# Kernel tuning notes

Measured on AMD Instinct MI355X. Metric: run time of the kernel, lower is better.

## Reference

```python
import jax, jax.numpy as jnp
import numpy as np

NUM_HEADS = 16
BLOCK_SIZE = 64


def setup_inputs() -> dict:
    key = jax.random.key(0)
    ks = jax.random.split(key, 5)
    B, S, C = 2, 2047, 1024
    return {
        "x": jax.random.normal(ks[0], (B, S, C), dtype=jnp.float32),
        "global_token": jax.random.normal(ks[1], (1, 1, C), dtype=jnp.float32),
        "qkv_w": jax.random.normal(ks[2], (3 * C, C), dtype=jnp.float32) * 0.02,
        "proj_w": jax.random.normal(ks[3], (C, C), dtype=jnp.float32) * 0.02,
        "proj_b": jax.random.normal(ks[4], (C,), dtype=jnp.float32) * 0.02,
    }


def reference(x, global_token, qkv_w, proj_w, proj_b):
    B, S, C = x.shape
    H = NUM_HEADS
    D = C // H
    scale = D ** -0.5
    # prepend global token -> N = S + 1
    g = jnp.broadcast_to(global_token, (B, 1, C))
    xg = jnp.concatenate([g, x], axis=1)
    N = S + 1
    # fused qkv projection (torch Linear: x @ W^T)
    qkv = (xg @ qkv_w.T).reshape(B, N, 3, H, D)
    qkv = jnp.transpose(qkv, (2, 0, 3, 1, 4))  # [3, B, H, N, D]
    q, k, v = qkv[0], qkv[1], qkv[2]
    # block-causal mask: query t sees key j iff block(j) <= block(t)
    blk = jnp.arange(N) // BLOCK_SIZE
    mask = blk[:, None] >= blk[None, :]  # [N, N]
    attn = jnp.einsum("bhqd,bhkd->bhqk", q, k) * scale
    attn = jnp.where(mask[None, None], attn, -jnp.inf)
    attn = jax.nn.softmax(attn, axis=-1)
    out = jnp.einsum("bhqk,bhkd->bhqd", attn, v)
    out = jnp.transpose(out, (0, 2, 1, 3)).reshape(B, N, C)
    out = out[:, 1:, :]  # drop global token
    return out @ proj_w.T + proj_b
```

## Files before the change

kernel.cpp:

```cpp
#include <hip/hip_runtime.h>
#include <math.h>

typedef _Float16 h16;
typedef _Float16 half8 __attribute__((ext_vector_type(8)));
typedef _Float16 half4 __attribute__((ext_vector_type(4)));
typedef float f32x4 __attribute__((ext_vector_type(4)));

#define NB 2
#define NS 2047
#define NC 1024
#define NN 2048
#define NH 16
#define ND 64

__device__ __forceinline__ void gl_lds16(const h16* g, h16* l) {
  __builtin_amdgcn_global_load_lds((const __attribute__((address_space(1))) void*)g,
                                   (__attribute__((address_space(3))) void*)l, 16, 0, 0);
}
__device__ __forceinline__ f32x4 mfma32(half8 a, half8 b, f32x4 c) {
  return __builtin_amdgcn_mfma_f32_16x16x32_f16(a, b, c, 0, 0, 0);
}
__device__ __forceinline__ f32x4 mfma16x(half4 a, half4 b, f32x4 c) {
  return __builtin_amdgcn_mfma_f32_16x16x16f16(a, b, c, 0, 0, 0);
}

__global__ __launch_bounds__(256) void cast_all_k(
    const float* __restrict__ x, const float* __restrict__ g,
    const float* __restrict__ qw, const float* __restrict__ pw, h16* __restrict__ out) {
  const size_t i = ((size_t)blockIdx.x * 256 + threadIdx.x) * 8;
  const float* src;
  if (i < (size_t)NB * NN * NC) {
    const int c = (int)(i & (NC - 1));
    const int n = (int)((i >> 10) & (NN - 1));
    const int b = (int)(i >> 21);
    src = (n == 0) ? (g + c) : (x + ((size_t)b * NS + (n - 1)) * NC + c);
  } else {
    const size_t j = i - (size_t)NB * NN * NC;
    src = (j < (size_t)3 * NC * NC) ? (qw + j) : (pw + (j - (size_t)3 * NC * NC));
  }
  float4 f0 = ((const float4*)src)[0];
  float4 f1 = ((const float4*)src)[1];
  h16 tmp[8];
  tmp[0] = (h16)f0.x; tmp[1] = (h16)f0.y; tmp[2] = (h16)f0.z; tmp[3] = (h16)f0.w;
  tmp[4] = (h16)f1.x; tmp[5] = (h16)f1.y; tmp[6] = (h16)f1.z; tmp[7] = (h16)f1.w;
  *(half8*)(out + i) = *(half8*)&tmp[0];
}

__global__ __launch_bounds__(256, 6) void gemm_qkv_h(
    const h16* __restrict__ A, const h16* __restrict__ W,
    h16* __restrict__ qP, h16* __restrict__ kP, h16* __restrict__ vP) {
  __shared__ h16 SM[64 * 64 + 128 * 64];
  h16* As = SM;
  h16* Bs = SM + 64 * 64;
  const int tid = threadIdx.x;
  const int flat = blockIdx.y * 24 + blockIdx.x;
  const int swz = (flat & 7) * 192 + (flat >> 3);
  const int m0 = (swz / 24) * 64, j0 = (swz % 24) * 128;
  const int wid = tid >> 6, lane = tid & 63, l15 = lane & 15, quad = lane >> 4;
  const int wr = wid >> 1, wc = wid & 1;
  const int rl = lane >> 3, csw = (lane & 7) ^ rl;
  const h16* ag0 = A + (size_t)(m0 + wid * 16 + rl) * NC + csw * 8;
  const h16* ag1 = A + (size_t)(m0 + wid * 16 + 8 + rl) * NC + csw * 8;
  const h16* bg = W + (size_t)(j0 + wid * 32 + rl) * NC + csw * 8;
  f32x4 acc[2][4];
#pragma unroll
  for (int rt = 0; rt < 2; ++rt)
#pragma unroll
    for (int ct = 0; ct < 4; ++ct) acc[rt][ct] = (f32x4){0.f, 0.f, 0.f, 0.f};

  for (int k0 = 0; k0 < NC; k0 += 64) {
    __syncthreads();
    gl_lds16(ag0 + k0, &As[(wid * 16) * 64]);
    gl_lds16(ag1 + k0, &As[(wid * 16 + 8) * 64]);
#pragma unroll
    for (int i = 0; i < 4; ++i)
      gl_lds16(bg + (size_t)i * 8 * NC + k0, &Bs[(wid * 32 + i * 8) * 64]);
    __syncthreads();
#pragma unroll
    for (int ks = 0; ks < 2; ++ks) {
      const int p0 = ((ks * 4 + quad) ^ (l15 & 7)) * 8;
      half8 af[2], bf[4];
#pragma unroll
      for (int rt = 0; rt < 2; ++rt)
        af[rt] = *(const half8*)&As[(wr * 32 + rt * 16 + l15) * 64 + p0];
#pragma unroll
      for (int ct = 0; ct < 4; ++ct)
        bf[ct] = *(const half8*)&Bs[(wc * 64 + ct * 16 + l15) * 64 + p0];
#pragma unroll
      for (int rt = 0; rt < 2; ++rt)
#pragma unroll
        for (int ct = 0; ct < 4; ++ct)
          acc[rt][ct] = mfma32(af[rt], bf[ct], acc[rt][ct]);
    }
  }

  const int b = m0 >> 11, n0 = m0 & (NN - 1);
  if (j0 < 2 * NC) {
    h16* base = (j0 < NC) ? qP : kP;
    const int coff = (j0 < NC) ? 0 : NC;
    const int h = (j0 - coff + wc * 64) >> 6;
    h16* dst = base + ((size_t)(b * NH + h) * NN + n0) * ND;
#pragma unroll
    for (int rt = 0; rt < 2; ++rt)
#pragma unroll
      for (int ct = 0; ct < 4; ++ct)
#pragma unroll
        for (int r = 0; r < 4; ++r) {
          const int mloc = wr * 32 + rt * 16 + quad * 4 + r;
          dst[(size_t)mloc * ND + ct * 16 + l15] = (h16)acc[rt][ct][r];
        }
  } else {
    __syncthreads();
#pragma unroll
    for (int rt = 0; rt < 2; ++rt)
#pragma unroll
      for (int ct = 0; ct < 4; ++ct)
#pragma unroll
        for (int r = 0; r < 4; ++r) {
          const int mloc = wr * 32 + rt * 16 + quad * 4 + r;
          const int jloc = wc * 64 + ct * 16 + l15;
          SM[mloc * 128 + (jloc ^ (((mloc >> 2) & 3) << 3))] = (h16)acc[rt][ct][r];
        }
    __syncthreads();
    const int kb0 = n0 >> 6;
    const int h0 = (j0 - 2 * NC) >> 6;
    const int w = tid >> 6, d = tid & 63;
#pragma unroll
    for (int u = 0; u < 2; ++u) {
      const int bh = b * NH + h0 + u;
      h16 buf[16];
#pragma unroll
      for (int kk = 0; kk < 16; ++kk) {
        const int row = w * 16 + kk;
        buf[kk] = SM[row * 128 + ((u * 64 + d) ^ (((row >> 2) & 3) << 3))];
      }
      h16* dstv = vP + ((size_t)((bh * 32 + kb0) * 4 + w)) * 1024 + d * 16;
      *(half8*)dstv = *(half8*)&buf[0];
      *(half8*)(dstv + 8) = *(half8*)&buf[8];
    }
  }
}

__global__ __launch_bounds__(256, 3) void attn_h(
    const h16* __restrict__ qP, const h16* __restrict__ kP,
    const h16* __restrict__ vP, h16* __restrict__ outp) {
  __shared__ float RED[2 * 64 * 36];
  __shared__ float DEN[4 * 64];
  const int bx = blockIdx.x;
  const int qb = 31 - (bx >> 5);
  const int bh = bx & 31;
  const int b = bh >> 4, h = bh & 15;
  const int tid = threadIdx.x, w = tid >> 6, lane = tid & 63;
  const int l15 = lane & 15, quad = lane >> 4;

  half8 bq[4][2];
#pragma unroll
  for (int nt = 0; nt < 4; ++nt) {
    const h16* qp = qP + ((size_t)bh * NN + qb * 64 + nt * 16 + l15) * ND + quad * 8;
    bq[nt][0] = (*(const half8*)qp) * (h16)0.125f;
    bq[nt][1] = (*(const half8*)(qp + 32)) * (h16)0.125f;
  }
  const h16* kbase = kP + ((size_t)bh * NN + w * 16 + l15) * ND + quad * 8;
  const h16* vbase = vP + ((size_t)bh * 32 * 4 + w) * 1024 + l15 * 16 + quad * 4;

  f32x4 o[4][4];
  float den[4] = {0.f, 0.f, 0.f, 0.f};
#pragma unroll
  for (int mt = 0; mt < 4; ++mt)
#pragma unroll
    for (int nt = 0; nt < 4; ++nt) o[mt][nt] = (f32x4){0.f, 0.f, 0.f, 0.f};

  half8 kf0 = *(const half8*)kbase;
  half8 kf1 = *(const half8*)(kbase + 32);
  half4 vf0 = *(const half4*)(vbase);
  half4 vf1 = *(const half4*)(vbase + 256);
  half4 vf2 = *(const half4*)(vbase + 512);
  half4 vf3 = *(const half4*)(vbase + 768);

  for (int kb = 0; kb <= qb; ++kb) {
    const int nkb = (kb < qb) ? kb + 1 : kb;
    const h16* kn = kbase + (size_t)nkb * 64 * ND;
    const h16* vn = vbase + (size_t)nkb * 4096;
    half8 nk0 = *(const half8*)kn;
    half8 nk1 = *(const half8*)(kn + 32);
    half4 nv0 = *(const half4*)(vn);
    half4 nv1 = *(const half4*)(vn + 256);
    half4 nv2 = *(const half4*)(vn + 512);
    half4 nv3 = *(const half4*)(vn + 768);
    __builtin_amdgcn_s_setprio(1);
#pragma unroll
    for (int nt = 0; nt < 4; ++nt) {
      f32x4 s = (f32x4){0.f, 0.f, 0.f, 0.f};
      s = mfma32(kf0, bq[nt][0], s);
      s = mfma32(kf1, bq[nt][1], s);
      float e0 = __expf(s[0]), e1 = __expf(s[1]);
      float e2 = __expf(s[2]), e3 = __expf(s[3]);
      den[nt] += (e0 + e1) + (e2 + e3);
      int2 pi;
      pi.x = __builtin_bit_cast(int, __builtin_amdgcn_cvt_pkrtz(e0, e1));
      pi.y = __builtin_bit_cast(int, __builtin_amdgcn_cvt_pkrtz(e2, e3));
      half4 p = __builtin_bit_cast(half4, pi);
      o[0][nt] = mfma16x(vf0, p, o[0][nt]);
      o[1][nt] = mfma16x(vf1, p, o[1][nt]);
      o[2][nt] = mfma16x(vf2, p, o[2][nt]);
      o[3][nt] = mfma16x(vf3, p, o[3][nt]);
    }
    __builtin_amdgcn_s_setprio(0);
    kf0 = nk0; kf1 = nk1;
    vf0 = nv0; vf1 = nv1; vf2 = nv2; vf3 = nv3;
  }

#pragma unroll
  for (int nt = 0; nt < 4; ++nt) {
    den[nt] += __shfl_xor(den[nt], 16);
    den[nt] += __shfl_xor(den[nt], 32);
  }
  __syncthreads();
  if (quad == 0) {
#pragma unroll
    for (int nt = 0; nt < 4; ++nt) DEN[w * 64 + nt * 16 + l15] = den[nt];
  }
#pragma unroll
  for (int r = 0; r < 2; ++r) {
    if (r) __syncthreads();
    if (w < 2) {
#pragma unroll
      for (int mt2 = 0; mt2 < 2; ++mt2)
#pragma unroll
        for (int nt = 0; nt < 4; ++nt)
          *(f32x4*)&RED[(w * 64 + nt * 16 + l15) * 36 + mt2 * 16 + quad * 4] =
              o[r * 2 + mt2][nt];
    }
    __syncthreads();
    if (w >= 2) {
#pragma unroll
      for (int mt2 = 0; mt2 < 2; ++mt2)
#pragma unroll
        for (int nt = 0; nt < 4; ++nt) {
          float* p = &RED[((w - 2) * 64 + nt * 16 + l15) * 36 + mt2 * 16 + quad * 4];
          f32x4 t = *(f32x4*)p;
          *(f32x4*)p = t + o[r * 2 + mt2][nt];
        }
    }
    __syncthreads();
    {
      const int q = w * 16 + l15;
      const float dt = DEN[q] + DEN[64 + q] + DEN[128 + q] + DEN[192 + q];
      const float inv = 1.f / dt;
      f32x4 x0 = *(const f32x4*)&RED[(0 * 64 + q) * 36 + quad * 8];
      f32x4 x1 = *(const f32x4*)&RED[(0 * 64 + q) * 36 + quad * 8 + 4];
      f32x4 y0 = *(const f32x4*)&RED[(1 * 64 + q) * 36 + quad * 8];
      f32x4 y1 = *(const f32x4*)&RED[(1 * 64 + q) * 36 + quad * 8 + 4];
      x0 += y0;
      x1 += y1;
      int4 pk;
      pk.x = __builtin_bit_cast(int, __builtin_amdgcn_cvt_pkrtz(x0[0] * inv, x0[1] * inv));
      pk.y = __builtin_bit_cast(int, __builtin_amdgcn_cvt_pkrtz(x0[2] * inv, x0[3] * inv));
      pk.z = __builtin_bit_cast(int, __builtin_amdgcn_cvt_pkrtz(x1[0] * inv, x1[1] * inv));
      pk.w = __builtin_bit_cast(int, __builtin_amdgcn_cvt_pkrtz(x1[2] * inv, x1[3] * inv));
      h16* op = outp + (size_t)(b * NN + qb * 64 + q) * NC + h * ND + r * 32 + quad * 8;
      *(half8*)op = __builtin_bit_cast(half8, pk);
    }
  }
}

__global__ __launch_bounds__(256) void gemm_proj_h(
    const h16* __restrict__ Ah, const h16* __restrict__ W,
    const float* __restrict__ bias, float* __restrict__ out) {
  __shared__ h16 As[64 * 64];
  __shared__ h16 Bs[128 * 64];
  const int tid = threadIdx.x;
  const int flat = blockIdx.y * 8 + blockIdx.x;
  const int swz = (flat & 7) * 64 + (flat >> 3);
  const int m0 = (swz >> 3) * 64, j0 = (swz & 7) * 128;
  const int wid = tid >> 6, lane = tid & 63, l15 = lane & 15, quad = lane >> 4;
  const int wr = wid >> 1, wc = wid & 1;
  const int rl = lane >> 3, csw = (lane & 7) ^ rl;
  const h16* ag[2];
#pragma unroll
  for (int i = 0; i < 2; ++i) {
    int m = m0 + wid * 16 + i * 8 + rl;
    if (m > NB * NS - 1) m = NB * NS - 1;
    const int bb = (m >= NS) ? 1 : 0;
    ag[i] = Ah + (size_t)(bb * NN + m - bb * NS + 1) * NC + csw * 8;
  }
  const h16* bg = W + (size_t)(j0 + wid * 32 + rl) * NC + csw * 8;
  f32x4 acc[2][4];
#pragma unroll
  for (int rt = 0; rt < 2; ++rt)
#pragma unroll
    for (int ct = 0; ct < 4; ++ct) acc[rt][ct] = (f32x4){0.f, 0.f, 0.f, 0.f};

  for (int k0 = 0; k0 < NC; k0 += 64) {
    __syncthreads();
    gl_lds16(ag[0] + k0, &As[(wid * 16) * 64]);
    gl_lds16(ag[1] + k0, &As[(wid * 16 + 8) * 64]);
#pragma unroll
    for (int i = 0; i < 4; ++i)
      gl_lds16(bg + (size_t)i * 8 * NC + k0, &Bs[(wid * 32 + i * 8) * 64]);
    __syncthreads();
#pragma unroll
    for (int ks = 0; ks < 2; ++ks) {
      const int p0 = ((ks * 4 + quad) ^ (l15 & 7)) * 8;
      half8 af[2], bf[4];
#pragma unroll
      for (int rt = 0; rt < 2; ++rt)
        af[rt] = *(const half8*)&As[(wr * 32 + rt * 16 + l15) * 64 + p0];
#pragma unroll
      for (int ct = 0; ct < 4; ++ct)
        bf[ct] = *(const half8*)&Bs[(wc * 64 + ct * 16 + l15) * 64 + p0];
#pragma unroll
      for (int rt = 0; rt < 2; ++rt)
#pragma unroll
        for (int ct = 0; ct < 4; ++ct)
          acc[rt][ct] = mfma32(af[rt], bf[ct], acc[rt][ct]);
    }
  }
#pragma unroll
  for (int ct = 0; ct < 4; ++ct) {
    const float bv = bias[j0 + wc * 64 + ct * 16 + l15];
#pragma unroll
    for (int rt = 0; rt < 2; ++rt)
#pragma unroll
      for (int r = 0; r < 4; ++r) {
        const int mm = m0 + wr * 32 + rt * 16 + quad * 4 + r;
        if (mm < NB * NS)
          out[(size_t)mm * NC + j0 + wc * 64 + ct * 16 + l15] = acc[rt][ct][r] + bv;
      }
  }
}

extern "C" void kernel_launch(void* const* d_in, const int* in_sizes, int n_in,
                              void* d_out, int out_size, void* d_ws, size_t ws_size,
                              hipStream_t stream) {
  const float* x = (const float*)d_in[0];
  const float* g = (const float*)d_in[1];
  const float* qkv_w = (const float*)d_in[2];
  const float* proj_w = (const float*)d_in[3];
  const float* proj_b = (const float*)d_in[4];
  float* out = (float*)d_out;

  h16* xgh  = (h16*)d_ws;
  h16* w3h  = xgh + (size_t)NB * NN * NC;
  h16* wph  = w3h + (size_t)3 * NC * NC;
  h16* qP   = wph + (size_t)NC * NC;
  h16* kP   = qP + (size_t)NB * NH * NN * ND;
  h16* vP   = kP + (size_t)NB * NH * NN * ND;
  h16* attnh = vP + (size_t)NB * NH * NN * ND;

  cast_all_k<<<dim3(4096), 256, 0, stream>>>(x, g, qkv_w, proj_w, xgh);
  gemm_qkv_h<<<dim3(24, 64), 256, 0, stream>>>(xgh, w3h, qP, kP, vP);
  attn_h<<<dim3(1024), 256, 0, stream>>>(qP, kP, vP, attnh);
  gemm_proj_h<<<dim3(8, 64), 256, 0, stream>>>(attnh, wph, proj_b, out);
}
```

Measured before the change: 173.6 us.

## Restructure QKV GEMM into 256x256 tiles with double-buffered LDS pipeline

Rewrites the QKV projection GEMM from 64x128 tiles on 256 threads to 256x256 tiles on 512 threads, with each wave computing a 128x64 sub-tile. K-slices of 32 are double-buffered in LDS, and the next slice is prefetched with global_load_lds interleaved between MFMA groups, using manual vmcnt waits, raw barriers and setprio. The goal is higher arithmetic intensity and overlap of loads with compute. In exchange the grid shrinks to 192 blocks, which may underfill the 256 CUs, and register pressure from 128 accumulator floats per thread rises. The V transpose epilogue is reworked in two passes through LDS.

```diff
diff --git a/kernel.cpp b/kernel.cpp
--- a/kernel.cpp
+++ b/kernel.cpp
@@ -46,97 +46,129 @@
   *(half8*)(out + i) = *(half8*)&tmp[0];
 }
 
-__global__ __launch_bounds__(256, 6) void gemm_qkv_h(
+__global__ __launch_bounds__(512, 2) void gemm_qkv_h(
     const h16* __restrict__ A, const h16* __restrict__ W,
     h16* __restrict__ qP, h16* __restrict__ kP, h16* __restrict__ vP) {
-  __shared__ h16 SM[64 * 64 + 128 * 64];
-  h16* As = SM;
-  h16* Bs = SM + 64 * 64;
+  __shared__ h16 SM[32768];
   const int tid = threadIdx.x;
-  const int flat = blockIdx.y * 24 + blockIdx.x;
-  const int swz = (flat & 7) * 192 + (flat >> 3);
-  const int m0 = (swz / 24) * 64, j0 = (swz % 24) * 128;
+  const int flat = blockIdx.y * 12 + blockIdx.x;
+  const int swz = (flat & 7) * 24 + (flat >> 3);
+  const int m0 = (swz / 12) * 256, j0 = (swz % 12) * 256;
   const int wid = tid >> 6, lane = tid & 63, l15 = lane & 15, quad = lane >> 4;
-  const int wr = wid >> 1, wc = wid & 1;
-  const int rl = lane >> 3, csw = (lane & 7) ^ rl;
-  const h16* ag0 = A + (size_t)(m0 + wid * 16 + rl) * NC + csw * 8;
-  const h16* ag1 = A + (size_t)(m0 + wid * 16 + 8 + rl) * NC + csw * 8;
-  const h16* bg = W + (size_t)(j0 + wid * 32 + rl) * NC + csw * 8;
-  f32x4 acc[2][4];
-#pragma unroll
-  for (int rt = 0; rt < 2; ++rt)
-#pragma unroll
-    for (int ct = 0; ct < 4; ++ct) acc[rt][ct] = (f32x4){0.f, 0.f, 0.f, 0.f};
-
-  for (int k0 = 0; k0 < NC; k0 += 64) {
-    __syncthreads();
-    gl_lds16(ag0 + k0, &As[(wid * 16) * 64]);
-    gl_lds16(ag1 + k0, &As[(wid * 16 + 8) * 64]);
-#pragma unroll
-    for (int i = 0; i < 4; ++i)
-      gl_lds16(bg + (size_t)i * 8 * NC + k0, &Bs[(wid * 32 + i * 8) * 64]);
-    __syncthreads();
-#pragma unroll
-    for (int ks = 0; ks < 2; ++ks) {
-      const int p0 = ((ks * 4 + quad) ^ (l15 & 7)) * 8;
-      half8 af[2], bf[4];
-#pragma unroll
-      for (int rt = 0; rt < 2; ++rt)
-        af[rt] = *(const half8*)&As[(wr * 32 + rt * 16 + l15) * 64 + p0];
-#pragma unroll
-      for (int ct = 0; ct < 4; ++ct)
-        bf[ct] = *(const half8*)&Bs[(wc * 64 + ct * 16 + l15) * 64 + p0];
-#pragma unroll
-      for (int rt = 0; rt < 2; ++rt)
-#pragma unroll
-        for (int ct = 0; ct < 4; ++ct)
-          acc[rt][ct] = mfma32(af[rt], bf[ct], acc[rt][ct]);
-    }
+  const int wm = wid >> 2, wn = wid & 3;
+
+  const int glin = (lane & 7) ^ (lane >> 3);
+  const int rowoff = glin >> 2, kg = glin & 3;
+  const int srow = (wid * 8 + (lane >> 3)) * 2 + rowoff;
+  const h16* ag = A + (size_t)(m0 + srow) * NC + kg * 8;
+  const h16* bg = W + (size_t)(j0 + srow) * NC + kg * 8;
+
+  const int rsw = l15 >> 1;
+  const int gs = (((l15 & 1) << 2) | quad) ^ rsw;
+  const int aoff = wm * 4096 + rsw * 64 + gs * 8;
+  const int boff = wn * 2048 + rsw * 64 + gs * 8;
+
+  f32x4 acc[8][4];
+#pragma unroll
+  for (int fm = 0; fm < 8; ++fm)
+#pragma unroll
+    for (int fn = 0; fn < 4; ++fn) acc[fm][fn] = (f32x4){0.f, 0.f, 0.f, 0.f};
+
+  gl_lds16(ag, &SM[(wid * 8) * 64]);
+  gl_lds16(ag + (size_t)128 * NC, &SM[(64 + wid * 8) * 64]);
+  gl_lds16(bg, &SM[16384 + (wid * 8) * 64]);
+  gl_lds16(bg + (size_t)128 * NC, &SM[16384 + (64 + wid * 8) * 64]);
+
+  for (int kt = 0; kt < 32; ++kt) {
+    const int cur = kt & 1, nxt = cur ^ 1;
+    const int k1 = (kt + 1) * 32;
+    const bool pre = (kt < 31);
+    const h16* Ab = SM + cur * 8192;
+    const h16* Bb = SM + 16384 + cur * 8192;
+
+    if (pre) {
+      gl_lds16(ag + k1, &SM[nxt * 8192 + (wid * 8) * 64]);
+      gl_lds16(ag + (size_t)128 * NC + k1, &SM[nxt * 8192 + (64 + wid * 8) * 64]);
+      asm volatile("s_waitcnt vmcnt(2)" ::: "memory");
+    } else {
+      asm volatile("s_waitcnt vmcnt(0)" ::: "memory");
+    }
+    asm volatile("s_barrier" ::: "memory");
+
+    half8 bf[4];
+#pragma unroll
+    for (int fn = 0; fn < 4; ++fn) bf[fn] = *(const half8*)&Bb[boff + fn * 512];
+
+#pragma unroll
+    for (int q = 0; q < 4; ++q) {
+      if (q == 1 && pre)
+        gl_lds16(bg + k1, &SM[16384 + nxt * 8192 + (wid * 8) * 64]);
+      if (q == 2 && pre)
+        gl_lds16(bg + (size_t)128 * NC + k1, &SM[16384 + nxt * 8192 + (64 + wid * 8) * 64]);
+      half8 af0 = *(const half8*)&Ab[aoff + (q * 2 + 0) * 512];
+      half8 af1 = *(const half8*)&Ab[aoff + (q * 2 + 1) * 512];
+      __builtin_amdgcn_s_setprio(1);
+#pragma unroll
+      for (int fn = 0; fn < 4; ++fn) {
+        acc[q * 2 + 0][fn] = mfma32(af0, bf[fn], acc[q * 2 + 0][fn]);
+        acc[q * 2 + 1][fn] = mfma32(af1, bf[fn], acc[q * 2 + 1][fn]);
+      }
+      __builtin_amdgcn_s_setprio(0);
+    }
+    asm volatile("s_barrier" ::: "memory");
   }
 
   const int b = m0 >> 11, n0 = m0 & (NN - 1);
   if (j0 < 2 * NC) {
     h16* base = (j0 < NC) ? qP : kP;
     const int coff = (j0 < NC) ? 0 : NC;
-    const int h = (j0 - coff + wc * 64) >> 6;
+    const int h = (j0 - coff + wn * 64) >> 6;
     h16* dst = base + ((size_t)(b * NH + h) * NN + n0) * ND;
 #pragma unroll
-    for (int rt = 0; rt < 2; ++rt)
-#pragma unroll
-      for (int ct = 0; ct < 4; ++ct)
+    for (int fm = 0; fm < 8; ++fm)
+#pragma unroll
+      for (int fn = 0; fn < 4; ++fn)
 #pragma unroll
         for (int r = 0; r < 4; ++r) {
-          const int mloc = wr * 32 + rt * 16 + quad * 4 + r;
-          dst[(size_t)mloc * ND + ct * 16 + l15] = (h16)acc[rt][ct][r];
+          const int mloc = wm * 128 + fm * 16 + quad * 4 + r;
+          dst[(size_t)mloc * ND + fn * 16 + l15] = (h16)acc[fm][fn][r];
         }
   } else {
-    __syncthreads();
-#pragma unroll
-    for (int rt = 0; rt < 2; ++rt)
-#pragma unroll
-      for (int ct = 0; ct < 4; ++ct)
-#pragma unroll
-        for (int r = 0; r < 4; ++r) {
-          const int mloc = wr * 32 + rt * 16 + quad * 4 + r;
-          const int jloc = wc * 64 + ct * 16 + l15;
-          SM[mloc * 128 + (jloc ^ (((mloc >> 2) & 3) << 3))] = (h16)acc[rt][ct][r];
-        }
-    __syncthreads();
     const int kb0 = n0 >> 6;
     const int h0 = (j0 - 2 * NC) >> 6;
-    const int w = tid >> 6, d = tid & 63;
-#pragma unroll
-    for (int u = 0; u < 2; ++u) {
-      const int bh = b * NH + h0 + u;
-      h16 buf[16];
-#pragma unroll
-      for (int kk = 0; kk < 16; ++kk) {
-        const int row = w * 16 + kk;
-        buf[kk] = SM[row * 128 + ((u * 64 + d) ^ (((row >> 2) & 3) << 3))];
+    const int g = tid >> 6, d = tid & 63;
+    __syncthreads();
+#pragma unroll
+    for (int p = 0; p < 2; ++p) {
+      if (p) __syncthreads();
+      if (wm == p) {
+#pragma unroll
+        for (int fm = 0; fm < 8; ++fm)
+#pragma unroll
+          for (int fn = 0; fn < 4; ++fn)
+#pragma unroll
+            for (int r = 0; r < 4; ++r) {
+              const int lrow = fm * 16 + quad * 4 + r;
+              const int col = wn * 64 + fn * 16 + l15;
+              SM[lrow * 256 + (col ^ ((lrow & 7) << 3))] = (h16)acc[fm][fn][r];
+            }
       }
-      h16* dstv = vP + ((size_t)((bh * 32 + kb0) * 4 + w)) * 1024 + d * 16;
-      *(half8*)dstv = *(half8*)&buf[0];
-      *(half8*)(dstv + 8) = *(half8*)&buf[8];
+      __syncthreads();
+#pragma unroll
+      for (int u = 0; u < 4; ++u) {
+        const int idx = g * 4 + u;
+        const int kbl2 = idx >> 4, hl = (idx >> 2) & 3, w4 = idx & 3;
+        const int bh = b * NH + h0 + hl;
+        h16 buf[16];
+#pragma unroll
+        for (int kk = 0; kk < 16; ++kk) {
+          const int lrow = kbl2 * 64 + w4 * 16 + kk;
+          buf[kk] = SM[lrow * 256 + ((hl * 64 + d) ^ ((lrow & 7) << 3))];
+        }
+        h16* dstv = vP + ((size_t)((bh * 32 + kb0 + p * 2 + kbl2) * 4 + w4)) * 1024 + d * 16;
+        *(half8*)dstv = *(half8*)&buf[0];
+        *(half8*)(dstv + 8) = *(half8*)&buf[8];
+      }
     }
   }
 }
@@ -349,7 +381,7 @@
   h16* attnh = vP + (size_t)NB * NH * NN * ND;
 
   cast_all_k<<<dim3(4096), 256, 0, stream>>>(x, g, qkv_w, proj_w, xgh);
-  gemm_qkv_h<<<dim3(24, 64), 256, 0, stream>>>(xgh, w3h, qP, kP, vP);
+  gemm_qkv_h<<<dim3(12, 16), 512, 0, stream>>>(xgh, w3h, qP, kP, vP);
   attn_h<<<dim3(1024), 256, 0, stream>>>(qP, kP, vP, attnh);
   gemm_proj_h<<<dim3(8, 64), 256, 0, stream>>>(attnh, wph, proj_b, out);
 }
```

Result: no change. 170.9 us (median of 2 runs) (-1.6%).
